# Performance work log

Hardware: AMD Instinct MI355X
Metric: run time of the kernel (lower is better)

The kernel has to match this reference:

```python
import jax, jax.numpy as jnp
import numpy as np

B, T, C, HEAD = 8, 2048, 1024, 64


def setup_inputs() -> dict:
    key = jax.random.key(0)
    kx, kq, kk, kv = jax.random.split(key, 4)
    x = jax.random.normal(kx, (B, T, C), dtype=jnp.float32)
    Wq = jax.random.normal(kq, (C, HEAD), dtype=jnp.float32) * (C ** -0.5)
    Wk = jax.random.normal(kk, (C, HEAD), dtype=jnp.float32) * (C ** -0.5)
    Wv = jax.random.normal(kv, (C, HEAD), dtype=jnp.float32) * (C ** -0.5)
    return {"x": x, "Wq": Wq, "Wk": Wk, "Wv": Wv}


def reference(x, Wq, Wk, Wv):
    # q,k,v: [B, T, H] via bias-free linear projections
    q = jnp.einsum('btc,ch->bth', x, Wq)
    k = jnp.einsum('btc,ch->bth', x, Wk)
    v = jnp.einsum('btc,ch->bth', x, Wv)
    scale = k.shape[-1] ** -0.5
    # scores: [B, T, T]
    scores = jnp.einsum('bqh,bkh->bqk', q, k) * scale
    Tq = x.shape[1]
    causal = jnp.tril(jnp.ones((Tq, Tq), dtype=bool))  # [T, T]
    scores = jnp.where(causal[None, :, :], scores, -jnp.inf)
    # softmax forced to fp32 in the original (autocast block)
    weight = jax.nn.softmax(scores.astype(jnp.float32), axis=-1)
    # dropout is identity in eval / p=0 deterministic baseline
    out = jnp.einsum('bqk,bkh->bqh', weight.astype(v.dtype), v)  # [B, T, H]
    return out
```

## Files before the change

### kernel.cpp

```cpp
#include <hip/hip_runtime.h>
#include <hip/hip_bf16.h>
#include <stdint.h>

#define NB 8
#define NT 2048
#define NC 1024
#define NH 64

typedef __attribute__((ext_vector_type(8))) short bf16x8;
typedef __attribute__((ext_vector_type(4))) float f32x4;

#define MFMA(a, b, c) __builtin_amdgcn_mfma_f32_16x16x32_bf16((a), (b), (c), 0, 0, 0)

static __device__ __forceinline__ short f2bf(float f) {
  union { float f; uint32_t u; } v; v.f = f;
  uint32_t r = v.u + 0x7FFFu + ((v.u >> 16) & 1u);
  return (short)(r >> 16);
}
static __device__ __forceinline__ float bf2f(short h) {
  union { uint32_t u; float f; } v; v.u = ((uint32_t)(uint16_t)h) << 16;
  return v.f;
}
static __device__ __forceinline__ void gload_lds16(const void* g, void* l) {
  __builtin_amdgcn_global_load_lds(
      (const __attribute__((address_space(1))) uint32_t*)g,
      (__attribute__((address_space(3))) uint32_t*)l, 16, 0, 0);
}

__global__ __launch_bounds__(256) void w_prep(const float* __restrict__ Wq,
                                              const float* __restrict__ Wk,
                                              const float* __restrict__ Wv,
                                              short* __restrict__ Wt) {
  __shared__ short tile[64][68];
  const int blk = blockIdx.x;
  const int mat = blk / 16;
  const int k0 = (blk % 16) * 64;
  const float* W = (mat == 0) ? Wq : (mat == 1) ? Wk : Wv;
  const float scale = (mat == 0) ? 0.125f * 1.44269504088896f : 1.0f;
  const int tid = threadIdx.x;
  {
    int kk = tid >> 2;
    int h0 = (tid & 3) * 16;
    const float* src = W + (size_t)(k0 + kk) * NH + h0;
#pragma unroll
    for (int i = 0; i < 16; ++i) tile[kk][h0 + i] = f2bf(src[i] * scale);
  }
  __syncthreads();
  {
    int j = tid >> 2;
    int kk0 = (tid & 3) * 16;
    bf16x8 t0, t1;
#pragma unroll
    for (int i = 0; i < 8; ++i) { t0[i] = tile[kk0 + i][j]; t1[i] = tile[kk0 + 8 + i][j]; }
    short* dst = Wt + (size_t)(mat * 64 + j) * NC + k0 + kk0;
    *(bf16x8*)dst = t0;
    *(bf16x8*)(dst + 8) = t1;
  }
}

__global__ __launch_bounds__(512) void qkv_proj(const float* __restrict__ x,
                                                const short* __restrict__ Wt,
                                                short* __restrict__ Qo,
                                                short* __restrict__ Ko,
                                                short* __restrict__ VTo) {
  __shared__ char lds_raw[2][32768];
  const int tid = threadIdx.x;
  const int lane = tid & 63;
  const int wave = tid >> 6;
  const int l15 = lane & 15;
  const int hi = lane >> 4;
  const int m0 = blockIdx.x * 32;
  const int wr = wave & 1;
  const int wc = wave >> 1;

  f32x4 acc[3];
#pragma unroll
  for (int f = 0; f < 3; ++f) acc[f] = (f32x4){0.f, 0.f, 0.f, 0.f};

  int xr, xc;
  {
    int off = tid * 16;
    int ol = off ^ (((off >> 8) & 7) << 4);
    xr = ol >> 8; xc = (ol >> 2) & 63;
  }
  int wrow[3], wcol[3];
#pragma unroll
  for (int i = 0; i < 3; ++i) {
    int off = i * 8192 + tid * 16;
    int ol = off ^ (((off >> 7) & 7) << 4);
    wrow[i] = ol >> 7; wcol[i] = (ol >> 1) & 63;
  }

#define STAGE(k0, buf)                                                          \
  {                                                                             \
    char* xsb_ = lds_raw[buf];                                                  \
    char* wtb_ = lds_raw[buf] + 8192;                                           \
    gload_lds16(x + (size_t)(m0 + xr) * NC + (k0) + xc, xsb_ + tid * 16);       \
    _Pragma("unroll")                                                           \
    for (int i = 0; i < 3; ++i)                                                 \
      gload_lds16(Wt + (size_t)wrow[i] * NC + (k0) + wcol[i],                   \
                  wtb_ + i * 8192 + tid * 16);                                  \
  }

  STAGE(0, 0);
  __syncthreads();
  int cur = 0;
  for (int t = 0; t < 16; ++t) {
    if (t + 1 < 16) STAGE((t + 1) * 64, cur ^ 1);
    const char* xsb = lds_raw[cur];
    const char* wtb = lds_raw[cur] + 8192;
    const int r = wr * 16 + l15;
#pragma unroll
    for (int s = 0; s < 2; ++s) {
      int o1 = (r * 256 + s * 128 + hi * 32) ^ ((r & 7) << 4);
      int o2 = (r * 256 + s * 128 + hi * 32 + 16) ^ ((r & 7) << 4);
      float4 q0 = *(const float4*)(xsb + o1);
      float4 q1 = *(const float4*)(xsb + o2);
      bf16x8 a;
      a[0] = f2bf(q0.x); a[1] = f2bf(q0.y); a[2] = f2bf(q0.z); a[3] = f2bf(q0.w);
      a[4] = f2bf(q1.x); a[5] = f2bf(q1.y); a[6] = f2bf(q1.z); a[7] = f2bf(q1.w);
#pragma unroll
      for (int f = 0; f < 3; ++f) {
        int c = wc * 48 + f * 16 + l15;
        int ob = (c * 128 + s * 64 + hi * 16) ^ ((c & 7) << 4);
        bf16x8 b = *(const bf16x8*)(wtb + ob);
        acc[f] = MFMA(a, b, acc[f]);
      }
    }
    __syncthreads();
    cur ^= 1;
  }
#undef STAGE

#pragma unroll
  for (int f = 0; f < 3; ++f) {
    int c = wc * 48 + f * 16 + l15;
    int mat = c >> 6, h = c & 63;
    if (mat < 2) {
      short* dst = (mat == 0) ? Qo : Ko;
#pragma unroll
      for (int r = 0; r < 4; ++r) {
        int t = m0 + wr * 16 + hi * 4 + r;
        dst[(size_t)t * NH + h] = f2bf(acc[f][r]);
      }
    } else {
      int bb = m0 >> 11;
      int t0 = (m0 & 2047) + wr * 16 + hi * 4;
      short4 v;
      v.x = f2bf(acc[f][0]); v.y = f2bf(acc[f][1]);
      v.z = f2bf(acc[f][2]); v.w = f2bf(acc[f][3]);
      *(short4*)(VTo + ((size_t)(bb * 64 + h)) * NT + t0) = v;
    }
  }
}

__global__ __launch_bounds__(256, 2) void attn_fused(const short* __restrict__ Q,
                                                     const short* __restrict__ K,
                                                     const short* __restrict__ Vt,
                                                     float* __restrict__ out) {
  __shared__ short PO[4][32][72];
  __shared__ float Ls[4][32];
  __shared__ short Vs[4][4096];

  const int tid = threadIdx.x;
  const int lane = tid & 63;
  const int wave = tid >> 6;
  const int l15 = lane & 15;
  const int hi = lane >> 4;
  const int kg = hi * 8;

  const int bid = blockIdx.x;
  const int half = bid >> 8;
  const int rr = bid & 255;
  const int b = rr >> 5;
  const int i = rr & 31;
  const int qt = (half == 0) ? (63 - i) : i;
  const int ktmax = qt >> 1;
  const int q0 = qt * 32;

  bf16x8 qf[2][2];
#pragma unroll
  for (int m = 0; m < 2; ++m)
#pragma unroll
    for (int s = 0; s < 2; ++s)
      qf[m][s] = *(const bf16x8*)(Q + ((size_t)b * NT + q0 + m * 16 + l15) * NH +
                                  s * 32 + kg);

  f32x4 oacc[2][4];
#pragma unroll
  for (int m = 0; m < 2; ++m)
#pragma unroll
    for (int f = 0; f < 4; ++f) oacc[m][f] = (f32x4){0.f, 0.f, 0.f, 0.f};
  float ps[2][4];
#pragma unroll
  for (int m = 0; m < 2; ++m)
#pragma unroll
    for (int r = 0; r < 4; ++r) ps[m][r] = 0.f;

#define LOAD_K(dst, kt_)                                                        \
  {                                                                             \
    const short* kb_ = K + ((size_t)b * NT + (kt_) * 64) * NH;                  \
    _Pragma("unroll") for (int n = 0; n < 4; ++n)                               \
    _Pragma("unroll") for (int s = 0; s < 2; ++s)                               \
      dst[n][s] = *(const bf16x8*)(kb_ + (n * 16 + l15) * NH + s * 32 + kg);    \
  }
#define STAGE_V(kt_)                                                            \
  {                                                                             \
    _Pragma("unroll") for (int iv = 0; iv < 8; ++iv) {                          \
      int h_ = iv * 8 + (lane >> 3);                                            \
      int sb_ = (((lane & 7) * 16) ^ ((h_ & 7) << 4)) >> 1;                     \
      gload_lds16(Vt + ((size_t)(b * 64 + h_)) * NT + (kt_) * 64 + sb_,         \
                  &Vs[wave][iv * 512]);                                         \
    }                                                                           \
  }

  int kt = wave;
  bf16x8 kf[4][2];
  if (kt <= ktmax) LOAD_K(kf, kt);

  for (; kt <= ktmax; kt += 4) {
    STAGE_V(kt);

    f32x4 S[2][4];
#pragma unroll
    for (int m = 0; m < 2; ++m)
#pragma unroll
      for (int n = 0; n < 4; ++n) {
        S[m][n] = (f32x4){0.f, 0.f, 0.f, 0.f};
        S[m][n] = MFMA(qf[m][0], kf[n][0], S[m][n]);
        S[m][n] = MFMA(qf[m][1], kf[n][1], S[m][n]);
      }

    bf16x8 kn[4][2];
    const bool more = (kt + 4) <= ktmax;
    if (more) LOAD_K(kn, kt + 4);

    if (kt == ktmax) {
#pragma unroll
      for (int m = 0; m < 2; ++m)
#pragma unroll
        for (int n = 0; n < 4; ++n)
#pragma unroll
          for (int r = 0; r < 4; ++r)
            if (kt * 64 + n * 16 + l15 > q0 + m * 16 + hi * 4 + r)
              S[m][n][r] = -INFINITY;
    }
#pragma unroll
    for (int m = 0; m < 2; ++m)
#pragma unroll
      for (int n = 0; n < 4; ++n)
#pragma unroll
        for (int r = 0; r < 4; ++r) {
          float p = __builtin_amdgcn_exp2f(S[m][n][r]);
          S[m][n][r] = p;
          ps[m][r] += p;
        }

#pragma unroll
    for (int m = 0; m < 2; ++m)
#pragma unroll
      for (int n = 0; n < 4; ++n)
#pragma unroll
        for (int r = 0; r < 4; ++r)
          PO[wave][m * 16 + hi * 4 + r][n * 16 + l15] = f2bf(S[m][n][r]);

    bf16x8 pa[2][2];
#pragma unroll
    for (int m = 0; m < 2; ++m)
#pragma unroll
      for (int s = 0; s < 2; ++s)
        pa[m][s] = *(const bf16x8*)&PO[wave][m * 16 + l15][s * 32 + kg];

    if (more) {
      asm volatile("s_waitcnt vmcnt(8)" ::: "memory");
    } else {
      asm volatile("s_waitcnt vmcnt(0)" ::: "memory");
    }
    __builtin_amdgcn_sched_barrier(0);

    bf16x8 vf[4][2];
#pragma unroll
    for (int f = 0; f < 4; ++f)
#pragma unroll
      for (int s = 0; s < 2; ++s) {
        int h_ = f * 16 + l15;
        int ob = h_ * 128 + (((s * 32 + kg) * 2) ^ ((h_ & 7) << 4));
        vf[f][s] = *(const bf16x8*)((const char*)&Vs[wave][0] + ob);
      }
#pragma unroll
    for (int m = 0; m < 2; ++m)
#pragma unroll
      for (int f = 0; f < 4; ++f) {
        oacc[m][f] = MFMA(pa[m][0], vf[f][0], oacc[m][f]);
        oacc[m][f] = MFMA(pa[m][1], vf[f][1], oacc[m][f]);
      }
    if (more) {
#pragma unroll
      for (int n = 0; n < 4; ++n)
#pragma unroll
        for (int s = 0; s < 2; ++s) kf[n][s] = kn[n][s];
    }
  }
#undef LOAD_K
#undef STAGE_V

#pragma unroll
  for (int d = 1; d < 16; d <<= 1)
#pragma unroll
    for (int m = 0; m < 2; ++m)
#pragma unroll
      for (int r = 0; r < 4; ++r) ps[m][r] += __shfl_xor(ps[m][r], d);

  if (l15 == 0) {
#pragma unroll
    for (int m = 0; m < 2; ++m)
#pragma unroll
      for (int r = 0; r < 4; ++r)
        Ls[wave][m * 16 + hi * 4 + r] = ps[m][r];
  }
#pragma unroll
  for (int m = 0; m < 2; ++m)
#pragma unroll
    for (int f = 0; f < 4; ++f)
#pragma unroll
      for (int r = 0; r < 4; ++r)
        PO[wave][m * 16 + hi * 4 + r][f * 16 + l15] = f2bf(oacc[m][f][r]);
  __syncthreads();

  {
    const int row = tid >> 3;
    const int c0 = (tid & 7) * 8;
    float L = 0.f;
    float o[8] = {0.f, 0.f, 0.f, 0.f, 0.f, 0.f, 0.f, 0.f};
#pragma unroll
    for (int w = 0; w < 4; ++w) {
      L += Ls[w][row];
      short4 v0 = *(const short4*)&PO[w][row][c0];
      short4 v1 = *(const short4*)&PO[w][row][c0 + 4];
      o[0] += bf2f(v0.x); o[1] += bf2f(v0.y); o[2] += bf2f(v0.z); o[3] += bf2f(v0.w);
      o[4] += bf2f(v1.x); o[5] += bf2f(v1.y); o[6] += bf2f(v1.z); o[7] += bf2f(v1.w);
    }
    float inv = 1.f / L;
    float* po = out + ((size_t)b * NT + q0 + row) * NH + c0;
    float4 r0 = {o[0] * inv, o[1] * inv, o[2] * inv, o[3] * inv};
    float4 r1 = {o[4] * inv, o[5] * inv, o[6] * inv, o[7] * inv};
    *(float4*)po = r0;
    *(float4*)(po + 4) = r1;
  }
}

extern "C" void kernel_launch(void* const* d_in, const int* in_sizes, int n_in,
                              void* d_out, int out_size, void* d_ws, size_t ws_size,
                              hipStream_t stream) {
  const float* x  = (const float*)d_in[0];
  const float* Wq = (const float*)d_in[1];
  const float* Wk = (const float*)d_in[2];
  const float* Wv = (const float*)d_in[3];
  float* out = (float*)d_out;

  char* ws = (char*)d_ws;
  short* Wt = (short*)ws;
  short* Qb = (short*)(ws + (size_t)(1 << 20));
  short* Kb = (short*)(ws + (size_t)(3 << 20));
  short* Vt = (short*)(ws + (size_t)(5 << 20));

  hipLaunchKernelGGL(w_prep, dim3(48), dim3(256), 0, stream, Wq, Wk, Wv, Wt);
  hipLaunchKernelGGL(qkv_proj, dim3(512), dim3(512), 0, stream, x, Wt, Qb, Kb, Vt);
  hipLaunchKernelGGL(attn_fused, dim3(512), dim3(256), 0, stream, Qb, Kb, Vt, out);
}
```

Measured before the change: 45.56 us.

## Triple-buffer QKV projection loads with vmcnt-based waits and single barrier

```diff
diff --git a/kernel.cpp b/kernel.cpp
--- a/kernel.cpp
+++ b/kernel.cpp
@@ -63,7 +63,8 @@
                                                 short* __restrict__ Qo,
                                                 short* __restrict__ Ko,
                                                 short* __restrict__ VTo) {
-  __shared__ char lds_raw[2][32768];
+  __shared__ char xbuf[3][8192];
+  __shared__ char wbuf[3][24576];
   const int tid = threadIdx.x;
   const int lane = tid & 63;
   const int wave = tid >> 6;
@@ -91,46 +92,53 @@
     wrow[i] = ol >> 7; wcol[i] = (ol >> 1) & 63;
   }
 
-#define STAGE(k0, buf)                                                          \
-  {                                                                             \
-    char* xsb_ = lds_raw[buf];                                                  \
-    char* wtb_ = lds_raw[buf] + 8192;                                           \
-    gload_lds16(x + (size_t)(m0 + xr) * NC + (k0) + xc, xsb_ + tid * 16);       \
-    _Pragma("unroll")                                                           \
+#define SX(t) gload_lds16(x + (size_t)(m0 + xr) * NC + (t) * 64 + xc,           \
+                          &xbuf[(t) % 3][tid * 16])
+#define SW(t)                                                                   \
+  { _Pragma("unroll")                                                           \
     for (int i = 0; i < 3; ++i)                                                 \
-      gload_lds16(Wt + (size_t)wrow[i] * NC + (k0) + wcol[i],                   \
-                  wtb_ + i * 8192 + tid * 16);                                  \
-  }
-
-  STAGE(0, 0);
-  __syncthreads();
-  int cur = 0;
+      gload_lds16(Wt + (size_t)wrow[i] * NC + (t) * 64 + wcol[i],               \
+                  &wbuf[(t) % 3][i * 8192 + tid * 16]); }
+
+  SX(0); SW(0);
+  SX(1); SW(1);
+
+#pragma unroll
   for (int t = 0; t < 16; ++t) {
-    if (t + 1 < 16) STAGE((t + 1) * 64, cur ^ 1);
-    const char* xsb = lds_raw[cur];
-    const char* wtb = lds_raw[cur] + 8192;
-    const int r = wr * 16 + l15;
-#pragma unroll
-    for (int s = 0; s < 2; ++s) {
-      int o1 = (r * 256 + s * 128 + hi * 32) ^ ((r & 7) << 4);
-      int o2 = (r * 256 + s * 128 + hi * 32 + 16) ^ ((r & 7) << 4);
-      float4 q0 = *(const float4*)(xsb + o1);
-      float4 q1 = *(const float4*)(xsb + o2);
-      bf16x8 a;
-      a[0] = f2bf(q0.x); a[1] = f2bf(q0.y); a[2] = f2bf(q0.z); a[3] = f2bf(q0.w);
-      a[4] = f2bf(q1.x); a[5] = f2bf(q1.y); a[6] = f2bf(q1.z); a[7] = f2bf(q1.w);
-#pragma unroll
-      for (int f = 0; f < 3; ++f) {
-        int c = wc * 48 + f * 16 + l15;
-        int ob = (c * 128 + s * 64 + hi * 16) ^ ((c & 7) << 4);
-        bf16x8 b = *(const bf16x8*)(wtb + ob);
-        acc[f] = MFMA(a, b, acc[f]);
-      }
-    }
-    __syncthreads();
-    cur ^= 1;
-  }
-#undef STAGE
+    if (t < 15) {
+      asm volatile("s_waitcnt vmcnt(4)" ::: "memory");
+    } else {
+      asm volatile("s_waitcnt vmcnt(0)" ::: "memory");
+    }
+    __builtin_amdgcn_sched_barrier(0);
+    __builtin_amdgcn_s_barrier();
+    __builtin_amdgcn_sched_barrier(0);
+    if (t + 2 < 16) { SX(t + 2); SW(t + 2); }
+    {
+      const char* xsb = xbuf[t % 3];
+      const char* wtb = wbuf[t % 3];
+      const int r = wr * 16 + l15;
+#pragma unroll
+      for (int s = 0; s < 2; ++s) {
+        int o1 = (r * 256 + s * 128 + hi * 32) ^ ((r & 7) << 4);
+        int o2 = (r * 256 + s * 128 + hi * 32 + 16) ^ ((r & 7) << 4);
+        float4 q0 = *(const float4*)(xsb + o1);
+        float4 q1 = *(const float4*)(xsb + o2);
+        bf16x8 a;
+        a[0] = f2bf(q0.x); a[1] = f2bf(q0.y); a[2] = f2bf(q0.z); a[3] = f2bf(q0.w);
+        a[4] = f2bf(q1.x); a[5] = f2bf(q1.y); a[6] = f2bf(q1.z); a[7] = f2bf(q1.w);
+#pragma unroll
+        for (int f = 0; f < 3; ++f) {
+          int c = wc * 48 + f * 16 + l15;
+          int ob = (c * 128 + s * 64 + hi * 16) ^ ((c & 7) << 4);
+          bf16x8 b = *(const bf16x8*)(wtb + ob);
+          acc[f] = MFMA(a, b, acc[f]);
+        }
+      }
+    }
+  }
+#undef SX
+#undef SW
 
 #pragma unroll
   for (int f = 0; f < 3; ++f) {
@@ -271,11 +279,7 @@
       for (int s = 0; s < 2; ++s)
         pa[m][s] = *(const bf16x8*)&PO[wave][m * 16 + l15][s * 32 + kg];
 
-    if (more) {
-      asm volatile("s_waitcnt vmcnt(8)" ::: "memory");
-    } else {
-      asm volatile("s_waitcnt vmcnt(0)" ::: "memory");
-    }
+    asm volatile("s_waitcnt vmcnt(0)" ::: "memory");
     __builtin_amdgcn_sched_barrier(0);
 
     bf16x8 vf[4][2];
```

New measurement: 57.76 us. 26.8% more time.
